# Optimization experiments

Measured on AMD Instinct MI355X. Metric: run time of the kernel, lower is better.

Reference implementation:

```python
import jax, jax.numpy as jnp
import numpy as np
import math

N_HEAD = 16
N_EMBD = 1024
HEAD_D = N_EMBD // N_HEAD
BASE = 10000


def rope(Y):
    # Y: [b, h, t, d]; positions start at 1 as in the torch code
    d = Y.shape[-1]
    t = Y.shape[-2]
    theta = BASE ** (-2.0 * jnp.arange(d // 2, dtype=Y.dtype) / d)
    theta2 = jnp.concatenate([theta, theta], axis=0)          # [d]
    pos = jnp.arange(1, t + 1, dtype=Y.dtype)                 # [t]
    C = pos[:, None] * theta2[None, :]                        # [t, d]
    cos, sin = jnp.cos(C), jnp.sin(C)
    Y2 = jnp.concatenate([-Y[..., d // 2:], Y[..., : d // 2]], axis=-1)
    return Y * cos + Y2 * sin


def setup_inputs() -> dict:
    key = jax.random.key(0)
    ks = jax.random.split(key, 9)
    s = 0.02
    x = jax.random.normal(ks[0], (4, 2048, N_EMBD), dtype=jnp.float32)
    Wq = jax.random.normal(ks[1], (N_EMBD, N_EMBD), dtype=jnp.float32) * s
    bq = jnp.zeros((N_EMBD,), dtype=jnp.float32)
    Wk = jax.random.normal(ks[2], (N_EMBD, N_EMBD), dtype=jnp.float32) * s
    bk = jnp.zeros((N_EMBD,), dtype=jnp.float32)
    Wv = jax.random.normal(ks[3], (N_EMBD, N_EMBD), dtype=jnp.float32) * s
    bv = jnp.zeros((N_EMBD,), dtype=jnp.float32)
    Wo = jax.random.normal(ks[4], (N_EMBD, N_EMBD), dtype=jnp.float32) * s
    bo = jnp.zeros((N_EMBD,), dtype=jnp.float32)
    return {"x": x, "Wq": Wq, "bq": bq, "Wk": Wk, "bk": bk,
            "Wv": Wv, "bv": bv, "Wo": Wo, "bo": bo}


def reference(x, Wq, bq, Wk, bk, Wv, bv, Wo, bo):
    b, t, _ = x.shape
    def split_heads(y):
        return y.reshape(b, t, N_HEAD, HEAD_D).transpose(0, 2, 1, 3)  # b h t d
    q = split_heads(x @ Wq.T + bq)
    k = split_heads(x @ Wk.T + bk)
    v = split_heads(x @ Wv.T + bv)
    q, k = rope(q), rope(k)
    scale = math.sqrt(HEAD_D)
    att = jnp.einsum('bhqd,bhkd->bhqk', q, k) / scale
    mask = jnp.tril(jnp.ones((t, t), dtype=bool))
    att = jnp.where(mask, att, -jnp.inf)
    att = jax.nn.softmax(att, axis=-1)
    y = jnp.einsum('bhqk,bhkd->bhqd', att, v)
    y = y.transpose(0, 2, 1, 3).reshape(b, t, N_EMBD)
    return y @ Wo.T + bo
```

## Files before the change

### kernel.cpp

```cpp
#include <hip/hip_runtime.h>
#include <hip/hip_bf16.h>
#include <cstdint>

typedef __attribute__((ext_vector_type(8))) short short8;
typedef __attribute__((ext_vector_type(4))) short short4v;
typedef __attribute__((ext_vector_type(4))) float f32x4;
typedef __attribute__((ext_vector_type(16))) float f32x16;
typedef __attribute__((ext_vector_type(4))) unsigned int u32x4;
typedef unsigned short ushort_t;
typedef unsigned int uint32;

#define DEVI static __device__ __forceinline__

DEVI ushort_t f2bf(float f){
  uint32 u = __builtin_bit_cast(uint32, f);
  u += 0x7FFFu + ((u >> 16) & 1u);
  return (ushort_t)(u >> 16);
}
DEVI float bf2f(ushort_t s){
  uint32 u = ((uint32)s) << 16;
  return __builtin_bit_cast(float, u);
}
DEVI uint32 cvtpk_bf16(float lo, float hi){
  uint32 r;
  asm("v_cvt_pk_bf16_f32 %0, %1, %2" : "=v"(r) : "v"(lo), "v"(hi));
  return r;
}
DEVI void plswap(uint32& a, uint32& b){
  asm("v_permlane32_swap_b32 %0, %1" : "+v"(a), "+v"(b));
}

typedef __attribute__((address_space(1))) const uint32 g_u32;
typedef __attribute__((address_space(3))) uint32 l_u32;
#define GL_LDS16(gp, lp) __builtin_amdgcn_global_load_lds((g_u32*)(gp), (l_u32*)(lp), 16, 0, 0)

#define MFMA16(a, b, c) __builtin_amdgcn_mfma_f32_16x16x32_bf16(a, b, c, 0, 0, 0)

__global__ __launch_bounds__(256) void convert_all(
    const float* __restrict__ x, const float* __restrict__ wq, const float* __restrict__ wk,
    const float* __restrict__ wv, const float* __restrict__ wo,
    ushort_t* __restrict__ xb, ushort_t* __restrict__ wqkv, ushort_t* __restrict__ wob){
  int bid = blockIdx.x;
  const float* src; ushort_t* dst; long base;
  if (bid < 4096){ src = x; dst = xb; base = (long)bid * 2048; }
  else {
    int r = bid - 4096; int sel = r >> 9; int o = r & 511;
    src = sel==0?wq: sel==1?wk: sel==2?wv: wo;
    dst = (sel<3) ? (wqkv + (long)sel * 1048576) : wob;
    base = (long)o * 2048;
  }
  long i = base + (long)threadIdx.x * 8;
  const float* p = src + i;
  float4 a = *(const float4*)p;
  float4 b = *(const float4*)(p + 4);
  short8 v;
  v[0]=(short)f2bf(a.x); v[1]=(short)f2bf(a.y); v[2]=(short)f2bf(a.z); v[3]=(short)f2bf(a.w);
  v[4]=(short)f2bf(b.x); v[5]=(short)f2bf(b.y); v[6]=(short)f2bf(b.z); v[7]=(short)f2bf(b.w);
  *(short8*)(dst + i) = v;
}

__global__ __launch_bounds__(256) void rope_table(float2* __restrict__ tab){
  const int idx = blockIdx.x * 256 + threadIdx.x;
  const int tok = idx >> 5, j = idx & 31;
  const float theta = exp2f(-(float)j * 0.4152410118609203f);
  const float ang = (float)(tok + 1) * theta;
  float s, c;
  sincosf(ang, &s, &c);
  tab[idx] = make_float2(c, s);
}

__global__ __launch_bounds__(512, 2) void gemm_qkv(
    const ushort_t* __restrict__ A, const ushort_t* __restrict__ Bw,
    const float* __restrict__ bq, const float* __restrict__ bk, const float* __restrict__ bv,
    const float2* __restrict__ tab,
    ushort_t* __restrict__ Qb, ushort_t* __restrict__ Kb, ushort_t* __restrict__ Vt){
  __shared__ __align__(16) ushort_t S[73728];
  const int tid = threadIdx.x;
  const int w = tid >> 6, l = tid & 63, lr = l & 15, lg = l >> 4;
  const int wm = w >> 1, wn = w & 1;
  const int bid = (blockIdx.x & 7) * 96 + (blockIdx.x >> 3);
  const int bm = bid / 24, bn = bid % 24;
  const int m0 = bm << 8, n0 = bn << 7;
  const int rbase = tid >> 2;
  const int swzk = (tid & 3) ^ ((tid >> 3) & 3);
  const ushort_t* aS = A  + (long)(m0 + rbase) * 1024 + swzk * 8;
  const ushort_t* bS = Bw + (long)(n0 + rbase) * 1024 + swzk * 8;
  const int slot = (lg ^ ((lr >> 1) & 3)) << 3;
  const int arow = wm * 64 + lr;
  const int brow = wn * 64 + lr;
  f32x4 acc[4][4] = {};

#define STGA(kk, t, bf_) do{ \
    const ushort_t* _s = aS + (long)(t)*64 + (kk)*32; \
    ushort_t* _d = &S[(bf_)*24576 + (kk)*8192 + tid*8]; \
    GL_LDS16(_s,          _d); \
    GL_LDS16(_s + 131072, _d + 4096); }while(0)
#define STGB(kk, t, bf_) do{ \
    GL_LDS16(bS + (long)(t)*64 + (kk)*32, \
             &S[(bf_)*24576 + 16384 + (kk)*4096 + tid*8]); }while(0)

  STGA(0,0,0); STGB(0,0,0); STGA(1,0,0); STGB(1,0,0);
  STGA(0,1,1); STGB(0,1,1); STGA(1,1,1); STGB(1,1,1);
  asm volatile("s_waitcnt vmcnt(6)" ::: "memory");
  __builtin_amdgcn_s_barrier();

  int buf = 0;
  for (int t = 0; t < 16; ++t){
    const int nstg = (buf >= 1) ? buf - 1 : 2;
    const ushort_t* SA = &S[buf * 24576];
    const ushort_t* SB = &S[buf * 24576 + 16384];
    short8 af[4], bfv[4];
#pragma unroll
    for (int mi = 0; mi < 4; ++mi) af[mi]  = *(const short8*)&SA[(arow + mi*16)*32 + slot];
#pragma unroll
    for (int nc = 0; nc < 4; ++nc) bfv[nc] = *(const short8*)&SB[(brow + nc*16)*32 + slot];
    if (t < 14){ STGA(0, t+2, nstg); STGB(0, t+2, nstg); }
    __builtin_amdgcn_s_barrier();
    __builtin_amdgcn_s_setprio(1);
#pragma unroll
    for (int mi = 0; mi < 4; ++mi)
#pragma unroll
      for (int nc = 0; nc < 4; ++nc)
        acc[mi][nc] = MFMA16(af[mi], bfv[nc], acc[mi][nc]);
    __builtin_amdgcn_s_setprio(0);
    __builtin_amdgcn_s_barrier();
#pragma unroll
    for (int mi = 0; mi < 4; ++mi) af[mi]  = *(const short8*)&SA[8192 + (arow + mi*16)*32 + slot];
#pragma unroll
    for (int nc = 0; nc < 4; ++nc) bfv[nc] = *(const short8*)&SB[4096 + (brow + nc*16)*32 + slot];
    if (t < 14){ STGA(1, t+2, nstg); STGB(1, t+2, nstg); }
    __builtin_amdgcn_s_barrier();
    __builtin_amdgcn_s_setprio(1);
#pragma unroll
    for (int mi = 0; mi < 4; ++mi)
#pragma unroll
      for (int nc = 0; nc < 4; ++nc)
        acc[mi][nc] = MFMA16(af[mi], bfv[nc], acc[mi][nc]);
    __builtin_amdgcn_s_setprio(0);
    if (t < 14)       asm volatile("s_waitcnt vmcnt(6)" ::: "memory");
    else if (t == 14) asm volatile("s_waitcnt vmcnt(0)" ::: "memory");
    __builtin_amdgcn_s_barrier();
    buf = (buf >= 2) ? 0 : buf + 1;
  }
#undef STGA
#undef STGB

  const int colX = n0 + (wn << 6);
  const int sel = colX >> 10;
  const int h = (colX >> 6) & 15;
  const int cB = (colX & 1023) + lr;
  if (sel < 2){
    ushort_t* dst = sel ? Kb : Qb;
    const float* bp = sel ? bk : bq;
    const float bvs[4] = {bp[cB], bp[cB+16], bp[cB+32], bp[cB+48]};
#pragma unroll
    for (int mi = 0; mi < 4; ++mi){
      const int row0 = m0 + (wm << 6) + mi*16 + lg*4;
#pragma unroll
      for (int i = 0; i < 4; ++i){
        const int r = row0 + i;
        const int b = r >> 11, tok = r & 2047;
#pragma unroll
        for (int nc = 0; nc < 2; ++nc){
          const int j = nc*16 + lr;
          const float2 cs = tab[tok*32 + j];
          const float v0 = acc[mi][nc][i]   + bvs[nc];
          const float v1 = acc[mi][nc+2][i] + bvs[nc+2];
          const long base = (((long)((b<<4) + h) * 2048 + tok) << 6) + j;
          dst[base]      = f2bf(v0 * cs.x - v1 * cs.y);
          dst[base + 32] = f2bf(v1 * cs.x + v0 * cs.y);
        }
      }
    }
  } else {
    const float bvs[4] = {bv[cB], bv[cB+16], bv[cB+32], bv[cB+48]};
#pragma unroll
    for (int mi = 0; mi < 4; ++mi){
      const int row0 = m0 + (wm << 6) + mi*16 + lg*4;
#pragma unroll
      for (int nc = 0; nc < 4; ++nc){
        const int d = nc*16 + lr;
#pragma unroll
        for (int i = 0; i < 4; ++i){
          const int r = row0 + i;
          const int b = r >> 11, tok = r & 2047;
          Vt[((long)((b<<4) + h) * 64 + d) * 2048 + tok] = f2bf(acc[mi][nc][i] + bvs[nc]);
        }
      }
    }
  }
}

__global__ __launch_bounds__(256) void gemm_out(
    const ushort_t* __restrict__ A, const ushort_t* __restrict__ Bw,
    const float* __restrict__ bias, float* __restrict__ Cout){
  __shared__ ushort_t As[4096];
  __shared__ ushort_t Bs[4096];
  const int tid = threadIdx.x, l = tid & 63, w = tid >> 6;
  const int lr = l & 15, lg = l >> 4;
  const int bid = (blockIdx.x & 7) * 64 + (blockIdx.x >> 3);
  const int bm = bid >> 3, bn = bid & 7;
  const int m0 = bm << 7, n0 = bn << 7;
  const int wm = (w >> 1) << 6, wn = (w & 1) << 6;
  f32x4 acc[4][4] = {};
  const ushort_t* aS = A + (long)(m0 + (tid >> 2)) * 1024 + (tid & 3) * 8;
  const ushort_t* bS = Bw + (long)(n0 + (tid >> 2)) * 1024 + (tid & 3) * 8;
  const long skip = (long)64 * 1024;
  for (int kt = 0; kt < 32; ++kt){
    GL_LDS16(aS,        &As[w * 512]);
    GL_LDS16(aS + skip, &As[2048 + w * 512]);
    GL_LDS16(bS,        &Bs[w * 512]);
    GL_LDS16(bS + skip, &Bs[2048 + w * 512]);
    aS += 32; bS += 32;
    __syncthreads();
    short8 af[4], bfr[4];
#pragma unroll
    for (int mi = 0; mi < 4; ++mi) af[mi]  = *(const short8*)&As[(wm + mi*16 + lr)*32 + lg*8];
#pragma unroll
    for (int ni = 0; ni < 4; ++ni) bfr[ni] = *(const short8*)&Bs[(wn + ni*16 + lr)*32 + lg*8];
#pragma unroll
    for (int mi = 0; mi < 4; ++mi)
#pragma unroll
      for (int ni = 0; ni < 4; ++ni)
        acc[mi][ni] = MFMA16(af[mi], bfr[ni], acc[mi][ni]);
    __syncthreads();
  }
  const int colBase = n0 + wn + lr;
#pragma unroll
  for (int mi = 0; mi < 4; ++mi){
    const int row0 = m0 + wm + mi*16 + lg*4;
#pragma unroll
    for (int ni = 0; ni < 4; ++ni){
      const int col = colBase + ni*16;
      const float bvv = bias[col];
#pragma unroll
      for (int i = 0; i < 4; ++i)
        Cout[(long)(row0 + i) * 1024 + col] = acc[mi][ni][i] + bvv;
    }
  }
}

__global__ __launch_bounds__(512, 4) void attn(
    const ushort_t* __restrict__ Qb, const ushort_t* __restrict__ Kb,
    const ushort_t* __restrict__ Vt, ushort_t* __restrict__ yb){
  __shared__ __align__(16) ushort_t Ks[2][2048];
  __shared__ __align__(16) ushort_t Vs[2][2048];
  const int tid = threadIdx.x;
  const int w = tid >> 6, l = tid & 63;
  const int lq = l & 31;
  const int hi = l >> 5;
  const int xcd = blockIdx.x & 7;
  const int idx = blockIdx.x >> 3;
  const int hi5 = idx >> 5;
  const int bh  = (xcd << 3) + ((idx >> 3) & 3) + hi5 * 4;
  const int qj  = hi5 ? (idx & 7) : 7 - (idx & 7);
  const int qc = (qj << 3) + w;
  const int q0 = qc << 5;
  const int ktmax = (qj << 3) + 7;
  const ushort_t* Qh = Qb + (long)bh * 2048 * 64;
  const ushort_t* Kh = Kb + (long)bh * 2048 * 64;
  const ushort_t* Vth = Vt + (long)bh * 64 * 2048;
  const int h8 = hi * 8;

  const ushort_t* qp = &Qh[(long)(q0 + lq) * 64 + h8];
  short8 qf0 = *(const short8*)(qp);
  short8 qf1 = *(const short8*)(qp + 16);
  short8 qf2 = *(const short8*)(qp + 32);
  short8 qf3 = *(const short8*)(qp + 48);

  const int stg_is_v = (w >= 4);
  long stg_src_off; int stg_dst_off;
  if (!stg_is_v){
    const int row = (w << 3) + (l >> 3);
    const int cl  = (l & 7) ^ (row & 7);
    stg_src_off = ((long)row << 6) + (cl << 3);
    stg_dst_off = (w << 9) + (l << 3);
  } else {
    const int row = ((w - 4) << 3) + (l >> 3);
    const int cl  = (l & 7) ^ (row & 7);
    const int dd  = row + ((cl & 4) << 3);
    stg_src_off = ((long)dd << 11) + ((cl & 3) << 3);
    stg_dst_off = ((w - 4) << 9) + (l << 3);
  }

  f32x16 o0 = {}, o1 = {};
  float lsum = 0.f;
  const float cl2 = 0.1803368801111204f;

  if (!stg_is_v) GL_LDS16(Kh + stg_src_off,  &Ks[0][stg_dst_off]);
  else           GL_LDS16(Vth + stg_src_off, &Vs[0][stg_dst_off]);
  __syncthreads();

  int cur = 0;
  for (int kt = 0; kt <= ktmax; ++kt){
    if (kt < ktmax){
      const int k0n = (kt + 1) << 5;
      if (!stg_is_v) GL_LDS16(Kh + ((long)k0n << 6) + stg_src_off, &Ks[cur ^ 1][stg_dst_off]);
      else           GL_LDS16(Vth + k0n + stg_src_off,             &Vs[cur ^ 1][stg_dst_off]);
    }
    if (kt <= qc){
      const int swk = lq & 7;
      const ushort_t* kr = &Ks[cur][lq << 6];
      short8 kf0 = *(const short8*)&kr[((hi    ) ^ swk) << 3];
      short8 kf1 = *(const short8*)&kr[((2 + hi) ^ swk) << 3];
      short8 kf2 = *(const short8*)&kr[((4 + hi) ^ swk) << 3];
      short8 kf3 = *(const short8*)&kr[((6 + hi) ^ swk) << 3];
      const ushort_t* vr = &Vs[cur][lq << 6];
      short8 vf00 = *(const short8*)&vr[((hi    ) ^ swk) << 3];
      short8 vf01 = *(const short8*)&vr[((2 + hi) ^ swk) << 3];
      short8 vf10 = *(const short8*)&vr[((4 + hi) ^ swk) << 3];
      short8 vf11 = *(const short8*)&vr[((6 + hi) ^ swk) << 3];
      f32x16 s = {};
      s = __builtin_amdgcn_mfma_f32_32x32x16_bf16(kf0, qf0, s, 0, 0, 0);
      s = __builtin_amdgcn_mfma_f32_32x32x16_bf16(kf1, qf1, s, 0, 0, 0);
      s = __builtin_amdgcn_mfma_f32_32x32x16_bf16(kf2, qf2, s, 0, 0, 0);
      s = __builtin_amdgcn_mfma_f32_32x32x16_bf16(kf3, qf3, s, 0, 0, 0);
      if (kt == qc){
#pragma unroll
        for (int r = 0; r < 16; ++r){
          const int rk = (r & 3) + 8 * (r >> 2) + 4 * hi;
          if (rk > lq) s[r] = -1e30f;
        }
      }
#pragma unroll
      for (int r = 0; r < 16; ++r) s[r] = __builtin_amdgcn_exp2f(__builtin_fmaf(s[r], cl2, -2.0f));
      {
        float t0 = (s[0] + s[1]) + (s[2] + s[3]);
        float t1 = (s[4] + s[5]) + (s[6] + s[7]);
        float t2 = (s[8] + s[9]) + (s[10] + s[11]);
        float t3 = (s[12] + s[13]) + (s[14] + s[15]);
        lsum += (t0 + t1) + (t2 + t3);
      }
      uint32 a0 = cvtpk_bf16(s[0], s[1]),  b0 = cvtpk_bf16(s[4], s[5]);
      uint32 a1 = cvtpk_bf16(s[2], s[3]),  b1 = cvtpk_bf16(s[6], s[7]);
      uint32 a2 = cvtpk_bf16(s[8], s[9]),  b2 = cvtpk_bf16(s[12], s[13]);
      uint32 a3 = cvtpk_bf16(s[10], s[11]),b3 = cvtpk_bf16(s[14], s[15]);
      plswap(a0, b0);
      plswap(a1, b1);
      plswap(a2, b2);
      plswap(a3, b3);
      u32x4 pc0 = {a0, a1, b0, b1};
      u32x4 pc1 = {a2, a3, b2, b3};
      short8 pb0 = __builtin_bit_cast(short8, pc0);
      short8 pb1 = __builtin_bit_cast(short8, pc1);
      o0 = __builtin_amdgcn_mfma_f32_32x32x16_bf16(vf00, pb0, o0, 0, 0, 0);
      o0 = __builtin_amdgcn_mfma_f32_32x32x16_bf16(vf01, pb1, o0, 0, 0, 0);
      o1 = __builtin_amdgcn_mfma_f32_32x32x16_bf16(vf10, pb0, o1, 0, 0, 0);
      o1 = __builtin_amdgcn_mfma_f32_32x32x16_bf16(vf11, pb1, o1, 0, 0, 0);
    }
    __syncthreads();
    cur ^= 1;
  }
  lsum += __shfl_xor(lsum, 32);
  const float inv = 1.0f / lsum;
  const int b = bh >> 4, h = bh & 15;
  const int tok = q0 + lq;
  ushort_t* yrow = yb + (long)(b * 2048 + tok) * 1024 + h * 64;
#pragma unroll
  for (int g = 0; g < 4; ++g){
    short4v p0, p1;
#pragma unroll
    for (int j = 0; j < 4; ++j){
      p0[j] = (short)f2bf(o0[4*g + j] * inv);
      p1[j] = (short)f2bf(o1[4*g + j] * inv);
    }
    *(short4v*)&yrow[8*g + 4*hi]      = p0;
    *(short4v*)&yrow[32 + 8*g + 4*hi] = p1;
  }
}

extern "C" void kernel_launch(void* const* d_in, const int* in_sizes, int n_in,
                              void* d_out, int out_size, void* d_ws, size_t ws_size,
                              hipStream_t stream){
  const float* x  = (const float*)d_in[0];
  const float* Wq = (const float*)d_in[1];
  const float* bq = (const float*)d_in[2];
  const float* Wk = (const float*)d_in[3];
  const float* bk = (const float*)d_in[4];
  const float* Wv = (const float*)d_in[5];
  const float* bv = (const float*)d_in[6];
  const float* Wo = (const float*)d_in[7];
  const float* bo = (const float*)d_in[8];
  char* ws = (char*)d_ws;
  ushort_t* xb   = (ushort_t*)(ws);
  ushort_t* wqkv = (ushort_t*)(ws + 16777216);
  ushort_t* wob  = (ushort_t*)(ws + 23068672);
  float2*   tab  = (float2*)  (ws + 25165824);
  ushort_t* Qb   = (ushort_t*)(ws + 25690112);
  ushort_t* Kb   = (ushort_t*)(ws + 42467328);
  ushort_t* Vt   = (ushort_t*)(ws + 59244544);
  ushort_t* yb   = xb;

  convert_all<<<6144, 256, 0, stream>>>(x, Wq, Wk, Wv, Wo, xb, wqkv, wob);
  rope_table<<<256, 256, 0, stream>>>(tab);
  gemm_qkv<<<768, 512, 0, stream>>>(xb, wqkv, bq, bk, bv, tab, Qb, Kb, Vt);
  attn<<<512, 512, 0, stream>>>(Qb, Kb, Vt, yb);
  gemm_out<<<512, 256, 0, stream>>>(yb, wob, bo, (float*)d_out);
}
```

Before: 165.3 us.

## Pipeline output GEMM with triple-buffered LDS, fuse rope table, remap tiles

The output projection GEMM is rewritten to match the QKV GEMM design: 256x128 tiles, 512 threads, a triple-buffered LDS pipeline with async global-to-LDS loads, swizzled slots, and setprio around the MFMA blocks. This replaces the single-buffered loop that synchronised twice per k-step. The rope table computation is folded into the convert kernel as extra blocks, which removes one launch. The QKV GEMM tile-to-XCD mapping is changed to group tiles for better L2 locality, and attention's __syncthreads calls are replaced with explicit vmcnt waits plus raw barriers so the prefetch can stay in flight.

New measurement: 160.5 us. 1.03x faster.

```diff
diff --git a/kernel.cpp b/kernel.cpp
--- a/kernel.cpp
+++ b/kernel.cpp
@@ -39,8 +39,19 @@
 __global__ __launch_bounds__(256) void convert_all(
     const float* __restrict__ x, const float* __restrict__ wq, const float* __restrict__ wk,
     const float* __restrict__ wv, const float* __restrict__ wo,
-    ushort_t* __restrict__ xb, ushort_t* __restrict__ wqkv, ushort_t* __restrict__ wob){
+    ushort_t* __restrict__ xb, ushort_t* __restrict__ wqkv, ushort_t* __restrict__ wob,
+    float2* __restrict__ tab){
   int bid = blockIdx.x;
+  if (bid >= 6144){
+    const int idx = (bid - 6144) * 256 + threadIdx.x;
+    const int tok = idx >> 5, j = idx & 31;
+    const float theta = exp2f(-(float)j * 0.4152410118609203f);
+    const float ang = (float)(tok + 1) * theta;
+    float s, c;
+    sincosf(ang, &s, &c);
+    tab[idx] = make_float2(c, s);
+    return;
+  }
   const float* src; ushort_t* dst; long base;
   if (bid < 4096){ src = x; dst = xb; base = (long)bid * 2048; }
   else {
@@ -57,16 +68,6 @@
   v[0]=(short)f2bf(a.x); v[1]=(short)f2bf(a.y); v[2]=(short)f2bf(a.z); v[3]=(short)f2bf(a.w);
   v[4]=(short)f2bf(b.x); v[5]=(short)f2bf(b.y); v[6]=(short)f2bf(b.z); v[7]=(short)f2bf(b.w);
   *(short8*)(dst + i) = v;
-}
-
-__global__ __launch_bounds__(256) void rope_table(float2* __restrict__ tab){
-  const int idx = blockIdx.x * 256 + threadIdx.x;
-  const int tok = idx >> 5, j = idx & 31;
-  const float theta = exp2f(-(float)j * 0.4152410118609203f);
-  const float ang = (float)(tok + 1) * theta;
-  float s, c;
-  sincosf(ang, &s, &c);
-  tab[idx] = make_float2(c, s);
 }
 
 __global__ __launch_bounds__(512, 2) void gemm_qkv(
@@ -78,8 +79,12 @@
   const int tid = threadIdx.x;
   const int w = tid >> 6, l = tid & 63, lr = l & 15, lg = l >> 4;
   const int wm = w >> 1, wn = w & 1;
-  const int bid = (blockIdx.x & 7) * 96 + (blockIdx.x >> 3);
-  const int bm = bid / 24, bn = bid % 24;
+  const int xcd = blockIdx.x & 7;
+  const int l9  = blockIdx.x >> 3;
+  const int bg  = l9 >> 5;
+  const int rem = l9 & 31;
+  const int bm  = ((xcd & 3) << 3) + (rem >> 2);
+  const int bn  = ((xcd >> 2) * 12) + (bg << 2) + (rem & 3);
   const int m0 = bm << 8, n0 = bn << 7;
   const int rbase = tid >> 2;
   const int swzk = (tid & 3) ^ ((tid >> 3) & 3);
@@ -191,51 +196,93 @@
   }
 }
 
-__global__ __launch_bounds__(256) void gemm_out(
+__global__ __launch_bounds__(512, 2) void gemm_out(
     const ushort_t* __restrict__ A, const ushort_t* __restrict__ Bw,
     const float* __restrict__ bias, float* __restrict__ Cout){
-  __shared__ ushort_t As[4096];
-  __shared__ ushort_t Bs[4096];
-  const int tid = threadIdx.x, l = tid & 63, w = tid >> 6;
-  const int lr = l & 15, lg = l >> 4;
-  const int bid = (blockIdx.x & 7) * 64 + (blockIdx.x >> 3);
-  const int bm = bid >> 3, bn = bid & 7;
-  const int m0 = bm << 7, n0 = bn << 7;
-  const int wm = (w >> 1) << 6, wn = (w & 1) << 6;
+  __shared__ __align__(16) ushort_t S[73728];
+  const int tid = threadIdx.x;
+  const int w = tid >> 6, l = tid & 63, lr = l & 15, lg = l >> 4;
+  const int wm = w >> 1, wn = w & 1;
+  const int xcd = blockIdx.x & 7;
+  const int l9  = blockIdx.x >> 3;
+  const int bm  = (xcd << 2) + (l9 >> 3);
+  const int bn  = l9 & 7;
+  const int m0 = bm << 8, n0 = bn << 7;
+  const int rbase = tid >> 2;
+  const int swzk = (tid & 3) ^ ((tid >> 3) & 3);
+  const ushort_t* aS = A  + (long)(m0 + rbase) * 1024 + swzk * 8;
+  const ushort_t* bS = Bw + (long)(n0 + rbase) * 1024 + swzk * 8;
+  const int slot = (lg ^ ((lr >> 1) & 3)) << 3;
+  const int arow = wm * 64 + lr;
+  const int brow = wn * 64 + lr;
   f32x4 acc[4][4] = {};
-  const ushort_t* aS = A + (long)(m0 + (tid >> 2)) * 1024 + (tid & 3) * 8;
-  const ushort_t* bS = Bw + (long)(n0 + (tid >> 2)) * 1024 + (tid & 3) * 8;
-  const long skip = (long)64 * 1024;
-  for (int kt = 0; kt < 32; ++kt){
-    GL_LDS16(aS,        &As[w * 512]);
-    GL_LDS16(aS + skip, &As[2048 + w * 512]);
-    GL_LDS16(bS,        &Bs[w * 512]);
-    GL_LDS16(bS + skip, &Bs[2048 + w * 512]);
-    aS += 32; bS += 32;
-    __syncthreads();
-    short8 af[4], bfr[4];
-#pragma unroll
-    for (int mi = 0; mi < 4; ++mi) af[mi]  = *(const short8*)&As[(wm + mi*16 + lr)*32 + lg*8];
-#pragma unroll
-    for (int ni = 0; ni < 4; ++ni) bfr[ni] = *(const short8*)&Bs[(wn + ni*16 + lr)*32 + lg*8];
+
+#define STGA(kk, t, bf_) do{ \
+    const ushort_t* _s = aS + (long)(t)*64 + (kk)*32; \
+    ushort_t* _d = &S[(bf_)*24576 + (kk)*8192 + tid*8]; \
+    GL_LDS16(_s,          _d); \
+    GL_LDS16(_s + 131072, _d + 4096); }while(0)
+#define STGB(kk, t, bf_) do{ \
+    GL_LDS16(bS + (long)(t)*64 + (kk)*32, \
+             &S[(bf_)*24576 + 16384 + (kk)*4096 + tid*8]); }while(0)
+
+  STGA(0,0,0); STGB(0,0,0); STGA(1,0,0); STGB(1,0,0);
+  STGA(0,1,1); STGB(0,1,1); STGA(1,1,1); STGB(1,1,1);
+  asm volatile("s_waitcnt vmcnt(6)" ::: "memory");
+  __builtin_amdgcn_s_barrier();
+
+  int buf = 0;
+  for (int t = 0; t < 16; ++t){
+    const int nstg = (buf >= 1) ? buf - 1 : 2;
+    const ushort_t* SA = &S[buf * 24576];
+    const ushort_t* SB = &S[buf * 24576 + 16384];
+    short8 af[4], bfv[4];
+#pragma unroll
+    for (int mi = 0; mi < 4; ++mi) af[mi]  = *(const short8*)&SA[(arow + mi*16)*32 + slot];
+#pragma unroll
+    for (int nc = 0; nc < 4; ++nc) bfv[nc] = *(const short8*)&SB[(brow + nc*16)*32 + slot];
+    if (t < 14){ STGA(0, t+2, nstg); STGB(0, t+2, nstg); }
+    __builtin_amdgcn_s_barrier();
+    __builtin_amdgcn_s_setprio(1);
 #pragma unroll
     for (int mi = 0; mi < 4; ++mi)
 #pragma unroll
-      for (int ni = 0; ni < 4; ++ni)
-        acc[mi][ni] = MFMA16(af[mi], bfr[ni], acc[mi][ni]);
-    __syncthreads();
-  }
-  const int colBase = n0 + wn + lr;
+      for (int nc = 0; nc < 4; ++nc)
+        acc[mi][nc] = MFMA16(af[mi], bfv[nc], acc[mi][nc]);
+    __builtin_amdgcn_s_setprio(0);
+    __builtin_amdgcn_s_barrier();
+#pragma unroll
+    for (int mi = 0; mi < 4; ++mi) af[mi]  = *(const short8*)&SA[8192 + (arow + mi*16)*32 + slot];
+#pragma unroll
+    for (int nc = 0; nc < 4; ++nc) bfv[nc] = *(const short8*)&SB[4096 + (brow + nc*16)*32 + slot];
+    if (t < 14){ STGA(1, t+2, nstg); STGB(1, t+2, nstg); }
+    __builtin_amdgcn_s_barrier();
+    __builtin_amdgcn_s_setprio(1);
+#pragma unroll
+    for (int mi = 0; mi < 4; ++mi)
+#pragma unroll
+      for (int nc = 0; nc < 4; ++nc)
+        acc[mi][nc] = MFMA16(af[mi], bfv[nc], acc[mi][nc]);
+    __builtin_amdgcn_s_setprio(0);
+    if (t < 14)       asm volatile("s_waitcnt vmcnt(6)" ::: "memory");
+    else if (t == 14) asm volatile("s_waitcnt vmcnt(0)" ::: "memory");
+    __builtin_amdgcn_s_barrier();
+    buf = (buf >= 2) ? 0 : buf + 1;
+  }
+#undef STGA
+#undef STGB
+
+  const int colBase = n0 + (wn << 6) + lr;
 #pragma unroll
   for (int mi = 0; mi < 4; ++mi){
-    const int row0 = m0 + wm + mi*16 + lg*4;
-#pragma unroll
-    for (int ni = 0; ni < 4; ++ni){
-      const int col = colBase + ni*16;
+    const int row0 = m0 + (wm << 6) + mi*16 + lg*4;
+#pragma unroll
+    for (int nc = 0; nc < 4; ++nc){
+      const int col = colBase + nc*16;
       const float bvv = bias[col];
 #pragma unroll
       for (int i = 0; i < 4; ++i)
-        Cout[(long)(row0 + i) * 1024 + col] = acc[mi][ni][i] + bvv;
+        Cout[(long)(row0 + i) * 1024 + col] = acc[mi][nc][i] + bvv;
     }
   }
 }
@@ -289,7 +336,8 @@
 
   if (!stg_is_v) GL_LDS16(Kh + stg_src_off,  &Ks[0][stg_dst_off]);
   else           GL_LDS16(Vth + stg_src_off, &Vs[0][stg_dst_off]);
-  __syncthreads();
+  asm volatile("s_waitcnt vmcnt(0)" ::: "memory");
+  __builtin_amdgcn_s_barrier();
 
   int cur = 0;
   for (int kt = 0; kt <= ktmax; ++kt){
@@ -297,7 +345,11 @@
       const int k0n = (kt + 1) << 5;
       if (!stg_is_v) GL_LDS16(Kh + ((long)k0n << 6) + stg_src_off, &Ks[cur ^ 1][stg_dst_off]);
       else           GL_LDS16(Vth + k0n + stg_src_off,             &Vs[cur ^ 1][stg_dst_off]);
-    }
+      asm volatile("s_waitcnt vmcnt(1)" ::: "memory");
+    } else {
+      asm volatile("s_waitcnt vmcnt(0)" ::: "memory");
+    }
+    __builtin_amdgcn_s_barrier();
     if (kt <= qc){
       const int swk = lq & 7;
       const ushort_t* kr = &Ks[cur][lq << 6];
@@ -348,7 +400,7 @@
       o1 = __builtin_amdgcn_mfma_f32_32x32x16_bf16(vf10, pb0, o1, 0, 0, 0);
       o1 = __builtin_amdgcn_mfma_f32_32x32x16_bf16(vf11, pb1, o1, 0, 0, 0);
     }
-    __syncthreads();
+    __builtin_amdgcn_s_barrier();
     cur ^= 1;
   }
   lsum += __shfl_xor(lsum, 32);
@@ -391,9 +443,8 @@
   ushort_t* Vt   = (ushort_t*)(ws + 59244544);
   ushort_t* yb   = xb;
 
-  convert_all<<<6144, 256, 0, stream>>>(x, Wq, Wk, Wv, Wo, xb, wqkv, wob);
-  rope_table<<<256, 256, 0, stream>>>(tab);
+  convert_all<<<6400, 256, 0, stream>>>(x, Wq, Wk, Wv, Wo, xb, wqkv, wob, tab);
   gemm_qkv<<<768, 512, 0, stream>>>(xb, wqkv, bq, bk, bv, tab, Qb, Kb, Vt);
   attn<<<512, 512, 0, stream>>>(Qb, Kb, Vt, yb);
-  gemm_out<<<512, 256, 0, stream>>>(yb, wob, bo, (float*)d_out);
-}
+  gemm_out<<<256, 512, 0, stream>>>(yb, wob, bo, (float*)d_out);
+}
```
